# Performance work log

Measured on AMD Instinct MI355X. Metric: run time of the kernel, lower is better.

Reference implementation:

```python
import jax, jax.numpy as jnp
import numpy as np

N = 1024      # params.input_dim (f1 is a square [N, N] similarity matrix)
TOPK = 16     # params.topk
B = 64        # hardcoded batch in the original reshape
W = 2 * N // B  # spatial width after reshape


def setup_inputs() -> dict:
    key = jax.random.key(0)
    k1, k2, k3 = jax.random.split(key, 3)
    f1 = jax.random.normal(k1, (N, N), dtype=jnp.float32)
    # Conv2d(in=N, out=N, kernel=(TOPK, 1)) weights, kaiming-ish scale
    conv_w = jax.random.normal(k2, (N, N, TOPK, 1), dtype=jnp.float32) * 0.01
    conv_b = jax.random.normal(k3, (N,), dtype=jnp.float32) * 0.01
    return {"f1": f1, "conv_w": conv_w, "conv_b": conv_b}


def reference(f1, conv_w, conv_b):
    # i = topk indices along last dim (largest, sorted) -> [N, TOPK]
    _, idx = jax.lax.top_k(f1, TOPK)
    # pos = f1[i]: gather rows of f1 by the topk column indices -> [N, TOPK, N]
    pos = f1[idx]
    # repeat_interleave(TOPK, dim=0).reshape(N, TOPK, -1) == each row tiled TOPK times
    rep = jnp.broadcast_to(f1[:, None, :], (N, TOPK, N))
    # cat on dim=2 -> [N, TOPK, 2N]; reshape to NCHW [B, N, TOPK, W]
    out = jnp.concatenate([rep, pos], axis=2).reshape(B, N, TOPK, W)
    # Conv2d kernel (TOPK, 1), VALID padding collapses H -> 1: [B, N, 1, W]
    y = jax.lax.conv_general_dilated(
        out, conv_w, window_strides=(1, 1), padding='VALID',
        dimension_numbers=('NCHW', 'OIHW', 'NCHW'))
    y = y + conv_b[None, :, None, None]
    return jax.nn.relu(y).reshape(N, -1)  # [N, B*W] = [N, 2N]
```

## Files before the change

kernel.cpp:

```cpp
#include <hip/hip_runtime.h>
#include <stdint.h>


#define NDIM 1024
#define TK   16
#define KPOS 8192
#define KREP 512
#define NCOL 2048

typedef unsigned short u16;
typedef uint32_t u32;
typedef u16   u16x8  __attribute__((ext_vector_type(8)));
typedef __bf16 bf16x8 __attribute__((ext_vector_type(8)));
typedef float  f32x4  __attribute__((ext_vector_type(4)));

__device__ __forceinline__ u16 f2bf(float x) {
    union { float f; unsigned u; } v; v.f = x;
    unsigned r = 0x7FFFu + ((v.u >> 16) & 1u);
    return (u16)((v.u + r) >> 16);
}

__device__ __forceinline__ void load_lds_16B(const u16* g, u16* l) {
    __builtin_amdgcn_global_load_lds(
        (__attribute__((address_space(1))) void*)(uintptr_t)g,
        (__attribute__((address_space(3))) void*)(unsigned)(uintptr_t)l,
        16, 0, 0);
}

#define PREP_TOPK 256
#define PREP_ZERO 2048
#define PREP_CONV 4096
#define PREP_W1   1024
#define PREP_F1T  256

__global__ __launch_bounds__(256) void prep_kernel(const float* __restrict__ f1,
                                                   const float* __restrict__ W,
                                                   int* __restrict__ idx,
                                                   u16* __restrict__ Wb,
                                                   u16* __restrict__ W1b,
                                                   u16* __restrict__ f1t,
                                                   float* __restrict__ out) {
    const int bid = blockIdx.x;
    const int t = threadIdx.x;
    if (bid < PREP_TOPK) {
        const int lane = t & 63;
        const int row  = bid * 4 + (t >> 6);
        float v[16];
        const float* src = f1 + row * NDIM + lane;
        #pragma unroll
        for (int j = 0; j < 16; ++j) v[j] = src[j * 64];
        for (int sel = 0; sel < TK; ++sel) {
            float best = -3.402823466e38f; int bg = 0x7fffffff;
            #pragma unroll
            for (int j = 0; j < 16; ++j)
                if (v[j] > best) { best = v[j]; bg = j * 64 + lane; }
            #pragma unroll
            for (int s = 1; s < 64; s <<= 1) {
                float ov = __shfl_xor(best, s);
                int   og = __shfl_xor(bg, s);
                if (ov > best || (ov == best && og < bg)) { best = ov; bg = og; }
            }
            if (lane == sel) idx[row * TK + sel] = bg;
            #pragma unroll
            for (int j = 0; j < 16; ++j)
                if (bg == j * 64 + lane) v[j] = -3.402823466e38f;
        }
    } else if (bid < PREP_TOPK + PREP_ZERO) {
        const int zb = bid - PREP_TOPK;
        f32x4 z = {0.f, 0.f, 0.f, 0.f};
        *(f32x4*)(out + (size_t)(zb * 256 + t) * 4) = z;
    } else if (bid < PREP_TOPK + PREP_ZERO + PREP_CONV) {
        const int tid = (bid - PREP_TOPK - PREP_ZERO) * 256 + t;
        const int o  = tid >> 10;
        const int r  = tid & 1023;
        const int kp0 = r * 8;
        const int ip  = r >> 1;
        const int kh0 = (r & 1) * 8;
        const int i = (ip >> 5) * 64 + ((ip >> 1) & 15) * 4 + (ip & 1) + 2;
        const float* src = W + (size_t)o * 16384 + i * 16 + kh0;
        float4 a = *(const float4*)(src);
        float4 b = *(const float4*)(src + 4);
        u16x8 ov;
        ov[0] = f2bf(a.x); ov[1] = f2bf(a.y); ov[2] = f2bf(a.z); ov[3] = f2bf(a.w);
        ov[4] = f2bf(b.x); ov[5] = f2bf(b.y); ov[6] = f2bf(b.z); ov[7] = f2bf(b.w);
        *(u16x8*)(Wb + (size_t)o * KPOS + kp0) = ov;
    } else if (bid < PREP_TOPK + PREP_ZERO + PREP_CONV + PREP_W1) {
        const int o = bid - PREP_TOPK - PREP_ZERO - PREP_CONV;
        const float* wrow = W + (size_t)o * 16384;
        #pragma unroll
        for (int h = 0; h < 2; ++h) {
            const int kr = h * 256 + t;
            const int nl = kr >> 5, q = (kr >> 4) & 1, kh = kr & 15;
            const float* base = wrow + (nl * 64 + q) * 16 + kh;
            float s = 0.f;
            #pragma unroll
            for (int tt = 0; tt < 16; ++tt) s += base[tt * 64];
            W1b[o * KREP + kr] = f2bf(s);
        }
    } else {
        const int gb = bid - PREP_TOPK - PREP_ZERO - PREP_CONV - PREP_W1;
        const int unit = t >> 5;
        const int w = t & 31;
        const int rq = gb * 8 + unit;
        const int row = rq >> 1, q = rq & 1;
        const float* src = f1 + row * NDIM + q * 512;
        const int swp = ((w >> 2) & 1) * 8;
        u16 tmp[16];
        #pragma unroll
        for (int kh = 0; kh < 16; ++kh)
            tmp[kh ^ swp] = f2bf(src[kh * 32 + w]);
        u16* dst = f1t + ((size_t)row * 2 + q) * 512 + w * 16;
        *(u16x8*)(dst)     = *(u16x8*)(tmp);
        *(u16x8*)(dst + 8) = *(u16x8*)(tmp + 8);
    }
}

#define BM 128
#define BN 128
#define BK 64

__global__ __launch_bounds__(256, 2) void gemm_kernel(const u16* __restrict__ Ap,
                                                      const u16* __restrict__ A1,
                                                      const u16* __restrict__ f1t,
                                                      const int* __restrict__ idx,
                                                      float* __restrict__ out) {
    __shared__ __align__(16) u16 As[2][BM * BK];
    __shared__ __align__(16) u16 Bs[2][16 * 512];
    __shared__ int idxL[256];
    const int f = blockIdx.x;
    int m, n, kb, kiters, astride;
    const u16* Ab;
    bool isPos;
    if (f < 512) {
        m = f >> 6; const int u = f & 63; n = u & 15;
        astride = KPOS; kb = (u >> 4) * 2048; kiters = 32; Ab = Ap; isPos = true;
    } else {
        const int g = f - 512; m = g >> 4; n = g & 15;
        astride = KREP; kb = 0; kiters = 8; Ab = A1; isPos = false;
    }
    const int t    = threadIdx.x;
    const int lane = t & 63;
    const int wave = t >> 6;
    const int wm   = (wave >> 1) * 64;
    const int wn   = (wave & 1) * 64;
    const int quad = lane >> 4;
    const int l16  = lane & 15;
    const int sw   = l16 & 7;
    const int o0 = m * BM;
    const int n0 = n * BN;
    const int nb0 = n * 4;
    const int nl0 = kb >> 9;

    if (isPos) {
        const int bl = t >> 6, nlz = (t >> 4) & 3, tt = t & 15;
        idxL[t] = idx[((nb0 + bl) * 16 + nl0 + nlz) * TK + tt];
    }

    f32x4 acc[4][4] = {};

    const int rA = t >> 3;
    const int c8 = t & 7;
    const int csw = (c8 ^ (rA & 7)) * 8;
    const u16* gA = Ab + (size_t)(o0 + rA) * astride + kb + csw;
    const int ipb = kb >> 4;

    auto stage = [&](int it, int nb) {
        const int k0 = it * BK;
        u16* lA = As[nb] + t * 8;
        #pragma unroll
        for (int c = 0; c < 4; ++c)
            load_lds_16B(gA + (size_t)(c * 32) * astride + k0, lA + c * 2048);
        const int ip = ipb + it * 4 + wave;
        const int qp = ip & 1;
        int rows[4];
        if (isPos) {
            const int nlz = (ip >> 5) & 3, tt = (ip >> 1) & 15;
            #pragma unroll
            for (int bl = 0; bl < 4; ++bl)
                rows[bl] = idxL[bl * 64 + nlz * 16 + tt];
        } else {
            const int r0 = ip >> 1;
            #pragma unroll
            for (int bl = 0; bl < 4; ++bl)
                rows[bl] = (nb0 + bl) * 16 + r0;
        }
        #pragma unroll
        for (int bl = 0; bl < 4; ++bl)
            load_lds_16B(f1t + ((size_t)rows[bl] * 2 + qp) * 512 + lane * 8,
                         Bs[nb] + (wave * 4 + bl) * 512);
    };

    __syncthreads();
    stage(0, 0);
    __syncthreads();

    #pragma unroll 2
    for (int it = 0; it < kiters; ++it) {
        const int cur = it & 1;
        if (it + 1 < kiters) stage(it + 1, 1 - cur);

        #pragma unroll
        for (int ks = 0; ks < 2; ++ks) {
            bf16x8 af[4], bfr[4];
            #pragma unroll
            for (int mt = 0; mt < 4; ++mt) {
                u16x8 bits = *(const u16x8*)(As[cur] + (wm + mt * 16 + l16) * BK
                                                + (((ks * 4 + quad) ^ sw) * 8));
                af[mt] = __builtin_bit_cast(bf16x8, bits);
            }
            const int ci2 = ks * 2 + (quad >> 1);
            const int qh  = quad & 1;
            #pragma unroll
            for (int nt = 0; nt < 4; ++nt) {
                const int nn = wn + nt * 16 + l16;
                const int blocf = nn >> 5, w = nn & 31;
                u16x8 bits = *(const u16x8*)(Bs[cur] + (ci2 * 4 + blocf) * 512 + w * 16
                                                + ((qh ^ ((w >> 2) & 1)) * 8));
                bfr[nt] = __builtin_bit_cast(bf16x8, bits);
            }
            #pragma unroll
            for (int mt = 0; mt < 4; ++mt)
                #pragma unroll
                for (int nt = 0; nt < 4; ++nt)
                    acc[mt][nt] = __builtin_amdgcn_mfma_f32_16x16x32_bf16(
                        af[mt], bfr[nt], acc[mt][nt], 0, 0, 0);
        }
        __syncthreads();
    }

    #pragma unroll
    for (int nt = 0; nt < 4; ++nt) {
        const int nn = n0 + wn + nt * 16 + l16;
        const int bb = nn >> 5, w = nn & 31;
        #pragma unroll
        for (int mt = 0; mt < 4; ++mt) {
            #pragma unroll
            for (int r = 0; r < 4; ++r) {
                const int o = o0 + wm + mt * 16 + quad * 4 + r;
                unsafeAtomicAdd(out + (size_t)(bb * 16 + (o >> 6)) * 2048
                                    + (o & 63) * 32 + w,
                                acc[mt][nt][r]);
            }
        }
    }
}

__global__ __launch_bounds__(256) void finalize_kernel(float* __restrict__ out,
                                                       const float* __restrict__ bias) {
    const int tid = blockIdx.x * 256 + threadIdx.x;
    const int f = tid * 4;
    const int o = ((f >> 11) & 15) * 64 + ((f & 2047) >> 5);
    const float bv = bias[o];
    float4 x = *(float4*)(out + f);
    x.x = fmaxf(x.x + bv, 0.f);
    x.y = fmaxf(x.y + bv, 0.f);
    x.z = fmaxf(x.z + bv, 0.f);
    x.w = fmaxf(x.w + bv, 0.f);
    *(float4*)(out + f) = x;
}

extern "C" void kernel_launch(void* const* d_in, const int* in_sizes, int n_in,
                              void* d_out, int out_size, void* d_ws, size_t ws_size,
                              hipStream_t stream) {
    const float* f1   = (const float*)d_in[0];
    const float* Wc   = (const float*)d_in[1];
    const float* bias = (const float*)d_in[2];
    float* out = (float*)d_out;

    int* idx = (int*)d_ws;
    u16* Wb  = (u16*)((char*)d_ws + 65536);
    u16* W1b = (u16*)((char*)d_ws + 16842752);
    u16* f1t = (u16*)((char*)d_ws + 17891328);

    prep_kernel<<<PREP_TOPK + PREP_ZERO + PREP_CONV + PREP_W1 + PREP_F1T,
                  256, 0, stream>>>(f1, Wc, idx, Wb, W1b, f1t, out);
    gemm_kernel<<<512 + 128, 256, 0, stream>>>(Wb, W1b, f1t, idx, out);
    finalize_kernel<<<(NDIM * NCOL) / (4 * 256), 256, 0, stream>>>(out, bias);
}
```

Baseline: 164.9 us.

## Load B operand fragments directly from global memory instead of staging through LDS

Drops the LDS double buffer for the gathered B tile. Each wave now reads its B fragments straight from global memory into registers at the start of every k-iteration, while A stays staged through LDS. Launch bounds rise to 4 blocks per SM to use the freed shared memory for higher occupancy. In exchange, B loads are no longer prefetched a stage ahead, so global latency sits on the critical path, and register pressure under the tighter launch bound may cause spills.

```diff
diff --git a/kernel.cpp b/kernel.cpp
--- a/kernel.cpp
+++ b/kernel.cpp
@@ -119,13 +119,12 @@
 #define BN 128
 #define BK 64
 
-__global__ __launch_bounds__(256, 2) void gemm_kernel(const u16* __restrict__ Ap,
+__global__ __launch_bounds__(256, 4) void gemm_kernel(const u16* __restrict__ Ap,
                                                       const u16* __restrict__ A1,
                                                       const u16* __restrict__ f1t,
                                                       const int* __restrict__ idx,
                                                       float* __restrict__ out) {
     __shared__ __align__(16) u16 As[2][BM * BK];
-    __shared__ __align__(16) u16 Bs[2][16 * 512];
     __shared__ int idxL[256];
     const int f = blockIdx.x;
     int m, n, kb, kiters, astride;
@@ -164,66 +163,56 @@
     const u16* gA = Ab + (size_t)(o0 + rA) * astride + kb + csw;
     const int ipb = kb >> 4;
 
-    auto stage = [&](int it, int nb) {
+    auto stageA = [&](int it, int nb) {
         const int k0 = it * BK;
         u16* lA = As[nb] + t * 8;
         #pragma unroll
         for (int c = 0; c < 4; ++c)
             load_lds_16B(gA + (size_t)(c * 32) * astride + k0, lA + c * 2048);
-        const int ip = ipb + it * 4 + wave;
-        const int qp = ip & 1;
-        int rows[4];
-        if (isPos) {
-            const int nlz = (ip >> 5) & 3, tt = (ip >> 1) & 15;
-            #pragma unroll
-            for (int bl = 0; bl < 4; ++bl)
-                rows[bl] = idxL[bl * 64 + nlz * 16 + tt];
-        } else {
-            const int r0 = ip >> 1;
-            #pragma unroll
-            for (int bl = 0; bl < 4; ++bl)
-                rows[bl] = (nb0 + bl) * 16 + r0;
-        }
-        #pragma unroll
-        for (int bl = 0; bl < 4; ++bl)
-            load_lds_16B(f1t + ((size_t)rows[bl] * 2 + qp) * 512 + lane * 8,
-                         Bs[nb] + (wave * 4 + bl) * 512);
     };
 
     __syncthreads();
-    stage(0, 0);
+    stageA(0, 0);
     __syncthreads();
 
-    #pragma unroll 2
     for (int it = 0; it < kiters; ++it) {
         const int cur = it & 1;
-        if (it + 1 < kiters) stage(it + 1, 1 - cur);
-
+        if (it + 1 < kiters) stageA(it + 1, 1 - cur);
+
+        bf16x8 bfr[2][4];
+        const int qh = quad & 1;
         #pragma unroll
         for (int ks = 0; ks < 2; ++ks) {
-            bf16x8 af[4], bfr[4];
+            const int ip = ipb + it * 4 + ks * 2 + (quad >> 1);
+            const int qp = ip & 1;
+            #pragma unroll
+            for (int nt = 0; nt < 4; ++nt) {
+                const int nn = wn + nt * 16 + l16;
+                const int bloc = nn >> 5, w = nn & 31;
+                int row;
+                if (isPos) row = idxL[bloc * 64 + ((ip >> 5) & 3) * 16 + ((ip >> 1) & 15)];
+                else       row = (nb0 + bloc) * 16 + (ip >> 1);
+                const u16* p = f1t + ((size_t)row * 2 + qp) * 512 + w * 16
+                                   + ((qh ^ ((w >> 2) & 1)) * 8);
+                bfr[ks][nt] = __builtin_bit_cast(bf16x8, *(const u16x8*)p);
+            }
+        }
+
+        #pragma unroll
+        for (int ks = 0; ks < 2; ++ks) {
+            bf16x8 af[4];
             #pragma unroll
             for (int mt = 0; mt < 4; ++mt) {
                 u16x8 bits = *(const u16x8*)(As[cur] + (wm + mt * 16 + l16) * BK
                                                 + (((ks * 4 + quad) ^ sw) * 8));
                 af[mt] = __builtin_bit_cast(bf16x8, bits);
             }
-            const int ci2 = ks * 2 + (quad >> 1);
-            const int qh  = quad & 1;
-            #pragma unroll
-            for (int nt = 0; nt < 4; ++nt) {
-                const int nn = wn + nt * 16 + l16;
-                const int blocf = nn >> 5, w = nn & 31;
-                u16x8 bits = *(const u16x8*)(Bs[cur] + (ci2 * 4 + blocf) * 512 + w * 16
-                                                + ((qh ^ ((w >> 2) & 1)) * 8));
-                bfr[nt] = __builtin_bit_cast(bf16x8, bits);
-            }
             #pragma unroll
             for (int mt = 0; mt < 4; ++mt)
                 #pragma unroll
                 for (int nt = 0; nt < 4; ++nt)
                     acc[mt][nt] = __builtin_amdgcn_mfma_f32_16x16x32_bf16(
-                        af[mt], bfr[nt], acc[mt][nt], 0, 0, 0);
+                        af[mt], bfr[ks][nt], acc[mt][nt], 0, 0, 0);
         }
         __syncthreads();
     }
```

Measured after the change: 177.2 us. +7.5%, slower.

## Merge rep GEMM tiles into pos split-K blocks and fuse weight prep

Applied to the files above, without the earlier changes.

Weight conversion to bf16 and the per-row summed rep weights are now computed in one block per output channel. Each thread reads a contiguous 64-float chunk and reduces with wave shuffles instead of strided loads. The separate 128 rep-GEMM blocks are folded into the 512 split-K pos blocks as two extra k-iterations each, which removes a tail wave of blocks and evens out per-block work. The zero-fill uses fewer blocks with more stores each, and the explicit unroll pragma on the main loop is dropped.

```diff
diff --git a/kernel.cpp b/kernel.cpp
--- a/kernel.cpp
+++ b/kernel.cpp
@@ -28,9 +28,8 @@
 }
 
 #define PREP_TOPK 256
-#define PREP_ZERO 2048
-#define PREP_CONV 4096
-#define PREP_W1   1024
+#define PREP_ZERO 512
+#define PREP_W    1024
 #define PREP_F1T  256
 
 __global__ __launch_bounds__(256) void prep_kernel(const float* __restrict__ f1,
@@ -68,37 +67,43 @@
     } else if (bid < PREP_TOPK + PREP_ZERO) {
         const int zb = bid - PREP_TOPK;
         f32x4 z = {0.f, 0.f, 0.f, 0.f};
-        *(f32x4*)(out + (size_t)(zb * 256 + t) * 4) = z;
-    } else if (bid < PREP_TOPK + PREP_ZERO + PREP_CONV) {
-        const int tid = (bid - PREP_TOPK - PREP_ZERO) * 256 + t;
-        const int o  = tid >> 10;
-        const int r  = tid & 1023;
-        const int kp0 = r * 8;
-        const int ip  = r >> 1;
-        const int kh0 = (r & 1) * 8;
-        const int i = (ip >> 5) * 64 + ((ip >> 1) & 15) * 4 + (ip & 1) + 2;
-        const float* src = W + (size_t)o * 16384 + i * 16 + kh0;
-        float4 a = *(const float4*)(src);
-        float4 b = *(const float4*)(src + 4);
-        u16x8 ov;
-        ov[0] = f2bf(a.x); ov[1] = f2bf(a.y); ov[2] = f2bf(a.z); ov[3] = f2bf(a.w);
-        ov[4] = f2bf(b.x); ov[5] = f2bf(b.y); ov[6] = f2bf(b.z); ov[7] = f2bf(b.w);
-        *(u16x8*)(Wb + (size_t)o * KPOS + kp0) = ov;
-    } else if (bid < PREP_TOPK + PREP_ZERO + PREP_CONV + PREP_W1) {
-        const int o = bid - PREP_TOPK - PREP_ZERO - PREP_CONV;
-        const float* wrow = W + (size_t)o * 16384;
-        #pragma unroll
-        for (int h = 0; h < 2; ++h) {
-            const int kr = h * 256 + t;
-            const int nl = kr >> 5, q = (kr >> 4) & 1, kh = kr & 15;
-            const float* base = wrow + (nl * 64 + q) * 16 + kh;
-            float s = 0.f;
-            #pragma unroll
-            for (int tt = 0; tt < 16; ++tt) s += base[tt * 64];
-            W1b[o * KREP + kr] = f2bf(s);
+        float* p = out + (size_t)zb * 4096 + t * 16;
+        #pragma unroll
+        for (int j = 0; j < 4; ++j) *(f32x4*)(p + j * 4) = z;
+    } else if (bid < PREP_TOPK + PREP_ZERO + PREP_W) {
+        const int o = bid - PREP_TOPK - PREP_ZERO;
+        const int nl = t >> 4, tt = t & 15;
+        const float* src = W + (size_t)o * 16384 + t * 64;
+        float v[64];
+        #pragma unroll
+        for (int j = 0; j < 16; ++j)
+            *(float4*)(v + j * 4) = *(const float4*)(src + j * 4);
+        u16* pd = Wb + (size_t)o * KPOS + (nl * 32 + tt * 2) * 16;
+        #pragma unroll
+        for (int j = 0; j < 4; ++j) {
+            u16x8 ov;
+            #pragma unroll
+            for (int e = 0; e < 8; ++e) ov[e] = f2bf(v[32 + j * 8 + e]);
+            *(u16x8*)(pd + j * 8) = ov;
+        }
+        float rv[32];
+        #pragma unroll
+        for (int j = 0; j < 32; ++j) rv[j] = v[j];
+        #pragma unroll
+        for (int s = 1; s < 16; s <<= 1)
+            #pragma unroll
+            for (int j = 0; j < 32; ++j) rv[j] += __shfl_xor(rv[j], s);
+        #pragma unroll
+        for (int j4 = 0; j4 < 4; ++j4) {
+            if (tt == j4) {
+                u16x8 ov;
+                #pragma unroll
+                for (int e = 0; e < 8; ++e) ov[e] = f2bf(rv[j4 * 8 + e]);
+                *(u16x8*)(W1b + o * KREP + nl * 32 + j4 * 8) = ov;
+            }
         }
     } else {
-        const int gb = bid - PREP_TOPK - PREP_ZERO - PREP_CONV - PREP_W1;
+        const int gb = bid - PREP_TOPK - PREP_ZERO - PREP_W;
         const int unit = t >> 5;
         const int w = t & 31;
         const int rq = gb * 8 + unit;
@@ -118,6 +123,7 @@
 #define BM 128
 #define BN 128
 #define BK 64
+#define KITERS 34
 
 __global__ __launch_bounds__(256, 2) void gemm_kernel(const u16* __restrict__ Ap,
                                                       const u16* __restrict__ A1,
@@ -128,16 +134,10 @@
     __shared__ __align__(16) u16 Bs[2][16 * 512];
     __shared__ int idxL[256];
     const int f = blockIdx.x;
-    int m, n, kb, kiters, astride;
-    const u16* Ab;
-    bool isPos;
-    if (f < 512) {
-        m = f >> 6; const int u = f & 63; n = u & 15;
-        astride = KPOS; kb = (u >> 4) * 2048; kiters = 32; Ab = Ap; isPos = true;
-    } else {
-        const int g = f - 512; m = g >> 4; n = g & 15;
-        astride = KREP; kb = 0; kiters = 8; Ab = A1; isPos = false;
-    }
+    const int m = f >> 6;
+    const int u = f & 63;
+    const int n = u & 15;
+    const int z = u >> 4;
     const int t    = threadIdx.x;
     const int lane = t & 63;
     const int wave = t >> 6;
@@ -149,9 +149,10 @@
     const int o0 = m * BM;
     const int n0 = n * BN;
     const int nb0 = n * 4;
-    const int nl0 = kb >> 9;
-
-    if (isPos) {
+    const int kb = z * 2048;
+    const int nl0 = z * 4;
+
+    {
         const int bl = t >> 6, nlz = (t >> 4) & 3, tt = t & 15;
         idxL[t] = idx[((nb0 + bl) * 16 + nl0 + nlz) * TK + tt];
     }
@@ -161,28 +162,36 @@
     const int rA = t >> 3;
     const int c8 = t & 7;
     const int csw = (c8 ^ (rA & 7)) * 8;
-    const u16* gA = Ab + (size_t)(o0 + rA) * astride + kb + csw;
-    const int ipb = kb >> 4;
+    const u16* gApos = Ap + (size_t)(o0 + rA) * KPOS + kb + csw;
+    const u16* gArep = A1 + (size_t)(o0 + rA) * KREP + z * 128 + csw;
+    const int ipbp = kb >> 4;
+    const int ipbr = z * 8;
 
     auto stage = [&](int it, int nb) {
-        const int k0 = it * BK;
         u16* lA = As[nb] + t * 8;
-        #pragma unroll
-        for (int c = 0; c < 4; ++c)
-            load_lds_16B(gA + (size_t)(c * 32) * astride + k0, lA + c * 2048);
-        const int ip = ipb + it * 4 + wave;
-        const int qp = ip & 1;
-        int rows[4];
-        if (isPos) {
+        int rows[4], qp;
+        if (it < 32) {
+            const int k0 = it * BK;
+            #pragma unroll
+            for (int c = 0; c < 4; ++c)
+                load_lds_16B(gApos + (size_t)(c * 32) * KPOS + k0, lA + c * 2048);
+            const int ip = ipbp + it * 4 + wave;
+            qp = ip & 1;
             const int nlz = (ip >> 5) & 3, tt = (ip >> 1) & 15;
             #pragma unroll
             for (int bl = 0; bl < 4; ++bl)
                 rows[bl] = idxL[bl * 64 + nlz * 16 + tt];
         } else {
-            const int r0 = ip >> 1;
+            const int k0 = (it - 32) * BK;
+            #pragma unroll
+            for (int c = 0; c < 4; ++c)
+                load_lds_16B(gArep + (size_t)(c * 32) * KREP + k0, lA + c * 2048);
+            const int ip = ipbr + (it - 32) * 4 + wave;
+            qp = ip & 1;
+            const int nlr = ip >> 1;
             #pragma unroll
             for (int bl = 0; bl < 4; ++bl)
-                rows[bl] = (nb0 + bl) * 16 + r0;
+                rows[bl] = (nb0 + bl) * 16 + nlr;
         }
         #pragma unroll
         for (int bl = 0; bl < 4; ++bl)
@@ -194,10 +203,9 @@
     stage(0, 0);
     __syncthreads();
 
-    #pragma unroll 2
-    for (int it = 0; it < kiters; ++it) {
+    for (int it = 0; it < KITERS; ++it) {
         const int cur = it & 1;
-        if (it + 1 < kiters) stage(it + 1, 1 - cur);
+        if (it + 1 < KITERS) stage(it + 1, 1 - cur);
 
         #pragma unroll
         for (int ks = 0; ks < 2; ++ks) {
@@ -272,8 +280,8 @@
     u16* W1b = (u16*)((char*)d_ws + 16842752);
     u16* f1t = (u16*)((char*)d_ws + 17891328);
 
-    prep_kernel<<<PREP_TOPK + PREP_ZERO + PREP_CONV + PREP_W1 + PREP_F1T,
+    prep_kernel<<<PREP_TOPK + PREP_ZERO + PREP_W + PREP_F1T,
                   256, 0, stream>>>(f1, Wc, idx, Wb, W1b, f1t, out);
-    gemm_kernel<<<512 + 128, 256, 0, stream>>>(Wb, W1b, f1t, idx, out);
+    gemm_kernel<<<512, 256, 0, stream>>>(Wb, W1b, f1t, idx, out);
     finalize_kernel<<<(NDIM * NCOL) / (4 * 256), 256, 0, stream>>>(out, bias);
 }
```

After: 172.8 us. +4.8%, slower.
